# Kernel tuning notes

Hardware: AMD Instinct MI355X
Metric: run time of the kernel (lower is better)

## Reference

```python
import jax, jax.numpy as jnp
import numpy as np

N, E, U, R = 20000, 200000, 32, 64
NTYPES = 95
CUTOFF = 5.0
LN_EPS = 1e-5


def _init_linear(key, fan_in, fan_out, bias=True, dtype=jnp.float32):
    kw, kb = jax.random.split(key)
    bound = 1.0 / np.sqrt(fan_in)
    W = jax.random.uniform(kw, (fan_in, fan_out), dtype, -bound, bound)
    if not bias:
        return W
    b = jax.random.uniform(kb, (fan_out,), dtype, -bound, bound)
    return W, b


def setup_inputs() -> dict:
    key = jax.random.key(0)
    ks = jax.random.split(key, 20)
    f = jnp.float32
    Wd1, bd1 = _init_linear(ks[6], R, U)
    Wd2, bd2 = _init_linear(ks[7], R, U)
    Wd3, bd3 = _init_linear(ks[8], R, U)
    Wemb2, bemb2 = _init_linear(ks[9], 2 * U, U)
    Wemb3, bemb3 = _init_linear(ks[10], R, U)
    Ws1, bs1 = _init_linear(ks[11], U, 2 * U)
    Ws2, bs2 = _init_linear(ks[12], 2 * U, 3 * U)
    return {
        "node_type": jax.random.randint(ks[0], (N,), 0, NTYPES),
        "edge_attr": jax.random.normal(ks[1], (E, R), f),
        "bond_dist": jax.random.uniform(ks[2], (E,), f, 0.1, CUTOFF),
        "bond_vec": jax.random.normal(ks[3], (E, 3), f),
        "src": jax.random.randint(ks[4], (E,), 0, N),
        "dst": jax.random.randint(ks[5], (E,), 0, N),
        "emb_table": jax.random.normal(ks[13], (NTYPES, U), f),
        "Wd1": Wd1, "bd1": bd1, "Wd2": Wd2, "bd2": bd2, "Wd3": Wd3, "bd3": bd3,
        "Wemb2": Wemb2, "bemb2": bemb2, "Wemb3": Wemb3, "bemb3": bemb3,
        "Wt0": _init_linear(ks[14], U, U, bias=False),
        "Wt1": _init_linear(ks[15], U, U, bias=False),
        "Wt2": _init_linear(ks[16], U, U, bias=False),
        "Ws1": Ws1, "bs1": bs1, "Ws2": Ws2, "bs2": bs2,
        "ln_g": jnp.ones((U,), f), "ln_b": jnp.zeros((U,), f),
    }


def reference(node_type, edge_attr, bond_dist, bond_vec, src, dst,
              emb_table, Wd1, bd1, Wd2, bd2, Wd3, bd3,
              Wemb2, bemb2, Wemb3, bemb3, Wt0, Wt1, Wt2,
              Ws1, bs1, Ws2, bs2, ln_g, ln_b):
    act = jax.nn.silu
    dt = edge_attr.dtype
    Z = emb_table[node_type]                                        # [N,U]
    # cosine cutoff
    C = 0.5 * (jnp.cos(jnp.pi * bond_dist / CUTOFF) + 1.0) * (bond_dist <= CUTOFF).astype(dt)
    W1 = (edge_attr @ Wd1 + bd1) * C[:, None]                       # [E,U]
    W2 = (edge_attr @ Wd2 + bd2) * C[:, None]
    W3 = (edge_attr @ Wd3 + bd3) * C[:, None]
    v = bond_vec / jnp.linalg.norm(bond_vec, axis=1, keepdims=True)  # [E,3]
    eye = jnp.eye(3, dtype=dt)
    zero = jnp.zeros_like(v[:, 0])
    # vector_to_skewtensor
    A = jnp.stack([zero, -v[:, 2], v[:, 1],
                   v[:, 2], zero, -v[:, 0],
                   -v[:, 1], v[:, 0], zero], axis=1).reshape(-1, 3, 3)
    # vector_to_symtensor (outer product is already symmetric)
    t = v[:, :, None] * v[:, None, :]                               # [E,3,3]
    S = t - (jnp.trace(t, axis1=-2, axis2=-1) / 3.0)[:, None, None] * eye
    # edge message: Zij = emb2([v_src, v_dst])
    Zij = jnp.concatenate([Z[src], Z[dst]], axis=1) @ Wemb2 + bemb2  # [E,U]
    fI = Zij * W1  # Zij * new_radial_tensor weights, fused (same math)
    fA = Zij * W2
    fS = Zij * W3
    Iedge = fI[:, :, None, None] * eye                              # [E,U,3,3]
    Aedge = fA[:, :, None, None] * A[:, None, :, :]
    Sedge = fS[:, :, None, None] * S[:, None, :, :]
    seg = lambda x: jax.ops.segment_sum(x, dst, num_segments=N)
    Ie, Ae, Se = seg(Iedge), seg(Aedge), seg(Sedge)                 # [N,U,3,3]
    # tensor_norm + LayerNorm
    nrm = jnp.sum((Ie + Ae + Se) ** 2, axis=(-2, -1))               # [N,U]
    mu = jnp.mean(nrm, axis=-1, keepdims=True)
    var = jnp.mean((nrm - mu) ** 2, axis=-1, keepdims=True)
    nrm = (nrm - mu) / jnp.sqrt(var + LN_EPS) * ln_g + ln_b
    # per-channel linear mixing of tensor components
    Ie = jnp.einsum('nuij,uv->nvij', Ie, Wt0)
    Ae = jnp.einsum('nuij,uv->nvij', Ae, Wt1)
    Se = jnp.einsum('nuij,uv->nvij', Se, Wt2)
    nrm = act(nrm @ Ws1 + bs1)
    nrm = act(nrm @ Ws2 + bs2)                                      # [N,3U]
    nrm = nrm.reshape(nrm.shape[0], U, 3)
    X = (nrm[..., 0, None, None] * Ie
         + nrm[..., 1, None, None] * Ae
         + nrm[..., 2, None, None] * Se)                            # [N,U,3,3]
    edge_feat = edge_attr @ Wemb3 + bemb3                           # [E,U]
    return X, edge_feat
```

## Files before the change

### kernel.cpp

```cpp
#include <hip/hip_runtime.h>


#define EPW 8

__device__ inline void atomAddF(float* p, float v) {
#if defined(__HIP_PLATFORM_AMD__)
    unsafeAtomicAdd(p, v);
#else
    atomicAdd(p, v);
#endif
}

__global__ void ptype_kernel(const float* __restrict__ emb,
                             const float* __restrict__ We2,
                             const float* __restrict__ be2,
                             float* __restrict__ Pt1, float* __restrict__ Pt2) {
    const int c = threadIdx.x & 31;
    const int t = blockIdx.x * 8 + (threadIdx.x >> 5);
    if (t < 95) {
        float p1 = 0.f, p2 = 0.f;
        for (int k = 0; k < 32; ++k) {
            const float z = emb[t * 32 + k];
            p1 = fmaf(z, We2[k * 32 + c], p1);
            p2 = fmaf(z, We2[(32 + k) * 32 + c], p2);
        }
        Pt1[t * 32 + c] = p1 + be2[c];
        Pt2[t * 32 + c] = p2;
    }
}

__global__ void prep_zero(const int* __restrict__ nt,
                          const float* __restrict__ Pt1, const float* __restrict__ Pt2,
                          float* __restrict__ acc,
                          float* __restrict__ P1, float* __restrict__ P2, int N) {
    const int i = blockIdx.x * 256 + threadIdx.x;
    if (i < N * 320) acc[i] = 0.0f;
    if (i < N * 32) {
        const int n = i >> 5, c = i & 31;
        const int t = nt[n];
        P1[i] = Pt1[t * 32 + c];
        P2[i] = Pt2[t * 32 + c];
    }
}

__global__ __launch_bounds__(256) void edge_kernel(
    const float* __restrict__ edge_attr,
    const float* __restrict__ bond_dist,
    const float* __restrict__ bond_vec,
    const int*   __restrict__ src,
    const int*   __restrict__ dst,
    const float* __restrict__ Wd1, const float* __restrict__ bd1,
    const float* __restrict__ Wd2, const float* __restrict__ bd2,
    const float* __restrict__ Wd3, const float* __restrict__ bd3,
    const float* __restrict__ We3, const float* __restrict__ be3,
    const float* __restrict__ P1,
    const float* __restrict__ P2,
    float* __restrict__ acc,
    float* __restrict__ efeat,
    int E)
{
    __shared__ float4 sX[4][8][16];

    const int tid  = threadIdx.x;
    const int lane = tid & 63;
    const int c    = lane & 31;
    const int h    = lane >> 5;
    const int wv   = tid >> 6;

    float w0r[32], w1r[32], w2r[32], w3r[32];
#pragma unroll
    for (int kk = 0; kk < 32; ++kk) {
        const int row = (h << 5) + kk;
        w0r[kk] = Wd1[row * 32 + c];
        w1r[kk] = Wd2[row * 32 + c];
        w2r[kk] = Wd3[row * 32 + c];
        w3r[kk] = We3[row * 32 + c];
    }
    const float bd1r = bd1[c], bd2r = bd2[c], bd3r = bd3[c], be3r = be3[c];

    float4 (*sXw)[16] = sX[wv];

    const int wid = (blockIdx.x * 256 + tid) >> 6;
    const int nw  = gridDim.x * 4;
    const int ngroups = (E + EPW - 1) / EPW;

    for (int g = wid; g < ngroups; g += nw) {
        const int base = g * EPW;

        int si4[4], di4[4];
        float dd[4], vx[4], vy[4], vz[4];
#pragma unroll
        for (int jj = 0; jj < 4; ++jj) {
            int e = base + jj + (h << 2); if (e >= E) e = E - 1;
            si4[jj] = src[e]; di4[jj] = dst[e];
            dd[jj]  = bond_dist[e];
            vx[jj]  = bond_vec[3 * (size_t)e + 0];
            vy[jj]  = bond_vec[3 * (size_t)e + 1];
            vz[jj]  = bond_vec[3 * (size_t)e + 2];
        }

        {
            int ea = base + (lane >> 4);     if (ea >= E) ea = E - 1;
            int eb = base + 4 + (lane >> 4); if (eb >= E) eb = E - 1;
            const float4 xa = *(const float4*)&edge_attr[(size_t)ea * 64 + (lane & 15) * 4];
            const float4 xb = *(const float4*)&edge_attr[(size_t)eb * 64 + (lane & 15) * 4];
            sXw[lane >> 4][lane & 15]     = xa;
            sXw[4 + (lane >> 4)][lane & 15] = xb;
        }

        float A0[EPW], A1[EPW], A2[EPW], A3[EPW];
#pragma unroll
        for (int j = 0; j < EPW; ++j) { A0[j] = 0.f; A1[j] = 0.f; A2[j] = 0.f; A3[j] = 0.f; }

#pragma unroll
        for (int kq = 0; kq < 8; ++kq) {
            const int k0 = kq * 4;
#pragma unroll
            for (int j = 0; j < EPW; ++j) {
                const float4 xq = sXw[j][(h << 3) + kq];
                A0[j] = fmaf(xq.x, w0r[k0 + 0], A0[j]);
                A0[j] = fmaf(xq.y, w0r[k0 + 1], A0[j]);
                A0[j] = fmaf(xq.z, w0r[k0 + 2], A0[j]);
                A0[j] = fmaf(xq.w, w0r[k0 + 3], A0[j]);
                A1[j] = fmaf(xq.x, w1r[k0 + 0], A1[j]);
                A1[j] = fmaf(xq.y, w1r[k0 + 1], A1[j]);
                A1[j] = fmaf(xq.z, w1r[k0 + 2], A1[j]);
                A1[j] = fmaf(xq.w, w1r[k0 + 3], A1[j]);
                A2[j] = fmaf(xq.x, w2r[k0 + 0], A2[j]);
                A2[j] = fmaf(xq.y, w2r[k0 + 1], A2[j]);
                A2[j] = fmaf(xq.z, w2r[k0 + 2], A2[j]);
                A2[j] = fmaf(xq.w, w2r[k0 + 3], A2[j]);
                A3[j] = fmaf(xq.x, w3r[k0 + 0], A3[j]);
                A3[j] = fmaf(xq.y, w3r[k0 + 1], A3[j]);
                A3[j] = fmaf(xq.z, w3r[k0 + 2], A3[j]);
                A3[j] = fmaf(xq.w, w3r[k0 + 3], A3[j]);
            }
        }

        float az4[4];
#pragma unroll
        for (int jj = 0; jj < 4; ++jj)
            az4[jj] = P1[(size_t)si4[jj] * 32 + c] + P2[(size_t)di4[jj] * 32 + c];

#pragma unroll
        for (int jj = 0; jj < 4; ++jj) {
            const float sd0 = h ? A0[jj] : A0[jj + 4];
            const float sd1 = h ? A1[jj] : A1[jj + 4];
            const float sd2 = h ? A2[jj] : A2[jj + 4];
            const float sd3 = h ? A3[jj] : A3[jj + 4];
            const float mn0 = h ? A0[jj + 4] : A0[jj];
            const float mn1 = h ? A1[jj + 4] : A1[jj];
            const float mn2 = h ? A2[jj + 4] : A2[jj];
            const float mn3 = h ? A3[jj + 4] : A3[jj];
            const float t0 = mn0 + __shfl_xor(sd0, 32);
            const float t1 = mn1 + __shfl_xor(sd1, 32);
            const float t2 = mn2 + __shfl_xor(sd2, 32);
            const float t3 = mn3 + __shfl_xor(sd3, 32);

            const int e = base + jj + 4 * h;
            const bool val = (e < E);

            const float d = dd[jj];
            const float C = (d <= 5.0f) ? 0.5f * (cosf(3.14159265358979323846f * d / 5.0f) + 1.0f) : 0.0f;
            float v0 = vx[jj], v1 = vy[jj], v2 = vz[jj];
            const float inv = 1.0f / sqrtf(v0 * v0 + v1 * v1 + v2 * v2);
            v0 *= inv; v1 *= inv; v2 *= inv;
            const float tr3 = (v0 * v0 + v1 * v1 + v2 * v2) * (1.0f / 3.0f);
            const float y00 = v0 * v0 - tr3, y11 = v1 * v1 - tr3, y22 = v2 * v2 - tr3;
            const float y01 = v0 * v1, y02 = v0 * v2, y12 = v1 * v2;

            const float az = az4[jj];
            const float a1v = t0 + bd1r;
            const float a2v = t1 + bd2r;
            const float a3v = t2 + bd3r;
            const float a4v = t3 + be3r;
            const float w1v = a1v * C, w2v = a2v * C, w3v = a3v * C;
            const float fI = az * w1v, fA = az * w2v, fS = az * w3v;

            if (val) {
                efeat[(size_t)e * 32 + c] = a4v;
                float* ap = acc + (size_t)di4[jj] * 320 + c;
                atomAddF(ap,       fI);
                atomAddF(ap + 32,  fA * v0);
                atomAddF(ap + 64,  fA * v1);
                atomAddF(ap + 96,  fA * v2);
                atomAddF(ap + 128, fS * y00);
                atomAddF(ap + 160, fS * y01);
                atomAddF(ap + 192, fS * y02);
                atomAddF(ap + 224, fS * y11);
                atomAddF(ap + 256, fS * y12);
                atomAddF(ap + 288, fS * y22);
            }
        }
    }
}

__global__ __launch_bounds__(256) void node_kernel(
    const float* __restrict__ acc,
    const float* __restrict__ Wt0, const float* __restrict__ Wt1, const float* __restrict__ Wt2,
    const float* __restrict__ Ws1, const float* __restrict__ bs1,
    const float* __restrict__ Ws2, const float* __restrict__ bs2,
    const float* __restrict__ lng, const float* __restrict__ lnb,
    float* __restrict__ xout,
    int N)
{
    __shared__ float4 wtp[32][32];
    __shared__ float2 ws1p[32][32];
    __shared__ float4 ws2p[64][32];
    __shared__ float4 accS4[8][32][3];
    __shared__ float2 sb1p[32];
    __shared__ float4 sb2p[32];
    __shared__ float  sg[32], sbv[32];

    const int tid = threadIdx.x;
    for (int i = tid; i < 1024; i += 256) {
        const int k = i >> 5, u = i & 31;
        wtp[k][u]  = make_float4(Wt0[i], Wt1[i], Wt2[i], 0.f);
        ws1p[k][u] = make_float2(Ws1[k * 64 + u], Ws1[k * 64 + 32 + u]);
    }
    for (int i = tid; i < 2048; i += 256) {
        const int k = i >> 5, u = i & 31;
        ws2p[k][u] = make_float4(Ws2[k * 96 + 3 * u], Ws2[k * 96 + 3 * u + 1],
                                 Ws2[k * 96 + 3 * u + 2], 0.f);
    }
    if (tid < 32) {
        sb1p[tid] = make_float2(bs1[tid], bs1[tid + 32]);
        sb2p[tid] = make_float4(bs2[3 * tid], bs2[3 * tid + 1], bs2[3 * tid + 2], 0.f);
        sg[tid] = lng[tid]; sbv[tid] = lnb[tid];
    }
    __syncthreads();

    const int hw = tid >> 5, u = tid & 31;
    const int stride = gridDim.x * 8;

    for (int n = blockIdx.x * 8 + hw; n < N; n += stride) {
        const float* ap = acc + (size_t)n * 320 + u;
        const float c0 = ap[0],   a0 = ap[32],  a1 = ap[64],  a2 = ap[96];
        const float s00 = ap[128], s01 = ap[160], s02 = ap[192];
        const float s11 = ap[224], s12 = ap[256], s22 = ap[288];

        accS4[hw][u][0] = make_float4(c0, a0, a1, a2);
        accS4[hw][u][1] = make_float4(s00, s01, s02, s11);
        accS4[hw][u][2] = make_float4(s12, s22, 0.f, 0.f);

        const float m00 = c0 + s00, m11 = c0 + s11, m22 = c0 + s22;
        float nrm = m00 * m00 + m11 * m11 + m22 * m22
                  + 2.0f * (s01 * s01 + a2 * a2 + s02 * s02 + a1 * a1 + s12 * s12 + a0 * a0);

        float sum = nrm;
#pragma unroll
        for (int o = 16; o >= 1; o >>= 1) sum += __shfl_xor(sum, o, 32);
        const float mu = sum * (1.0f / 32.0f);
        const float dv = nrm - mu;
        float vs = dv * dv;
#pragma unroll
        for (int o = 16; o >= 1; o >>= 1) vs += __shfl_xor(vs, o, 32);
        const float var = vs * (1.0f / 32.0f);
        const float nl = dv * rsqrtf(var + 1e-5f) * sg[u] + sbv[u];

        const float2 b1 = sb1p[u];
        float h1a = b1.x, h1b = b1.y;
#pragma unroll
        for (int k = 0; k < 32; ++k) {
            const float x = __shfl(nl, k, 32);
            const float2 wq = ws1p[k][u];
            h1a = fmaf(x, wq.x, h1a);
            h1b = fmaf(x, wq.y, h1b);
        }
        h1a = h1a / (1.0f + __expf(-h1a));
        h1b = h1b / (1.0f + __expf(-h1b));

        const float4 b2 = sb2p[u];
        float f0 = b2.x, f1 = b2.y, f2 = b2.z;
#pragma unroll
        for (int k = 0; k < 32; ++k) {
            const float hh = __shfl(h1a, k, 32);
            const float4 wq = ws2p[k][u];
            f0 = fmaf(hh, wq.x, f0);
            f1 = fmaf(hh, wq.y, f1);
            f2 = fmaf(hh, wq.z, f2);
        }
#pragma unroll
        for (int k = 0; k < 32; ++k) {
            const float hh = __shfl(h1b, k, 32);
            const float4 wq = ws2p[32 + k][u];
            f0 = fmaf(hh, wq.x, f0);
            f1 = fmaf(hh, wq.y, f1);
            f2 = fmaf(hh, wq.z, f2);
        }
        f0 = f0 / (1.0f + __expf(-f0));
        f1 = f1 / (1.0f + __expf(-f1));
        f2 = f2 / (1.0f + __expf(-f2));

        float m0 = 0, ma0 = 0, ma1 = 0, ma2 = 0;
        float ms00 = 0, ms01 = 0, ms02 = 0, ms11 = 0, ms12 = 0, ms22 = 0;
#pragma unroll
        for (int k = 0; k < 32; ++k) {
            const float4 w  = wtp[k][u];
            const float4 q0 = accS4[hw][k][0];
            const float4 q1 = accS4[hw][k][1];
            const float4 q2 = accS4[hw][k][2];
            m0   = fmaf(q0.x, w.x, m0);
            ma0  = fmaf(q0.y, w.y, ma0);
            ma1  = fmaf(q0.z, w.y, ma1);
            ma2  = fmaf(q0.w, w.y, ma2);
            ms00 = fmaf(q1.x, w.z, ms00);
            ms01 = fmaf(q1.y, w.z, ms01);
            ms02 = fmaf(q1.z, w.z, ms02);
            ms11 = fmaf(q1.w, w.z, ms11);
            ms12 = fmaf(q2.x, w.z, ms12);
            ms22 = fmaf(q2.y, w.z, ms22);
        }

        float* xp = xout + (size_t)n * 288 + u * 9;
        xp[0] = f0 * m0 + f2 * ms00;
        xp[1] = f1 * (-ma2) + f2 * ms01;
        xp[2] = f1 * ( ma1) + f2 * ms02;
        xp[3] = f1 * ( ma2) + f2 * ms01;
        xp[4] = f0 * m0 + f2 * ms11;
        xp[5] = f1 * (-ma0) + f2 * ms12;
        xp[6] = f1 * (-ma1) + f2 * ms02;
        xp[7] = f1 * ( ma0) + f2 * ms12;
        xp[8] = f0 * m0 + f2 * ms22;
    }
}

extern "C" void kernel_launch(void* const* d_in, const int* in_sizes, int n_in,
                              void* d_out, int out_size, void* d_ws, size_t ws_size,
                              hipStream_t stream) {
    const int N = in_sizes[0];
    const int E = in_sizes[2];

    float* acc = (float*)d_ws;
    float* P1  = acc + (size_t)N * 320;
    float* P2  = P1 + (size_t)N * 32;
    float* Pt1 = P2 + (size_t)N * 32;
    float* Pt2 = Pt1 + 95 * 32;

    float* xout  = (float*)d_out;
    float* efeat = xout + (size_t)N * 288;

    ptype_kernel<<<12, 256, 0, stream>>>(
        (const float*)d_in[6], (const float*)d_in[13], (const float*)d_in[14], Pt1, Pt2);

    prep_zero<<<(N * 320 + 255) / 256, 256, 0, stream>>>(
        (const int*)d_in[0], Pt1, Pt2, acc, P1, P2, N);

    edge_kernel<<<768, 256, 0, stream>>>(
        (const float*)d_in[1], (const float*)d_in[2], (const float*)d_in[3],
        (const int*)d_in[4], (const int*)d_in[5],
        (const float*)d_in[7],  (const float*)d_in[8],
        (const float*)d_in[9],  (const float*)d_in[10],
        (const float*)d_in[11], (const float*)d_in[12],
        (const float*)d_in[15], (const float*)d_in[16],
        P1, P2, acc, efeat, E);

    node_kernel<<<512, 256, 0, stream>>>(
        acc,
        (const float*)d_in[17], (const float*)d_in[18], (const float*)d_in[19],
        (const float*)d_in[20], (const float*)d_in[21],
        (const float*)d_in[22], (const float*)d_in[23],
        (const float*)d_in[24], (const float*)d_in[25],
        xout, N);
}
```

Measured before the change: 429.1 us.

## Replace atomic scatter with CSR binning by destination and fused per-node kernel

Builds a CSR index of edges grouped by destination node (histogram, single-wave scan, atomic binning into a permutation). A fused kernel then assigns one wave per node, computes that node's incoming edges and reduces them in registers, and runs the norm/MLP/mixing stage directly. This removes the 10 float atomics per edge-channel, the accumulator zeroing, and the accumulator round trip through global memory. In exchange it adds a serial single-wave scan over 20k nodes, gathered edge_attr loads through the permutation, and load imbalance from variable node degree, with partially empty 8-edge groups wasting work on low-degree nodes.

```diff
diff --git a/kernel.cpp b/kernel.cpp
--- a/kernel.cpp
+++ b/kernel.cpp
@@ -2,14 +2,6 @@
 
 
 #define EPW 8
-
-__device__ inline void atomAddF(float* p, float v) {
-#if defined(__HIP_PLATFORM_AMD__)
-    unsafeAtomicAdd(p, v);
-#else
-    atomicAdd(p, v);
-#endif
-}
 
 __global__ void ptype_kernel(const float* __restrict__ emb,
                              const float* __restrict__ We2,
@@ -29,12 +21,12 @@
     }
 }
 
-__global__ void prep_zero(const int* __restrict__ nt,
-                          const float* __restrict__ Pt1, const float* __restrict__ Pt2,
-                          float* __restrict__ acc,
-                          float* __restrict__ P1, float* __restrict__ P2, int N) {
+__global__ void prep_kernel(const int* __restrict__ nt,
+                            const float* __restrict__ Pt1, const float* __restrict__ Pt2,
+                            float* __restrict__ P1, float* __restrict__ P2,
+                            int* __restrict__ hist, int N) {
     const int i = blockIdx.x * 256 + threadIdx.x;
-    if (i < N * 320) acc[i] = 0.0f;
+    if (i < N) hist[i] = 0;
     if (i < N * 32) {
         const int n = i >> 5, c = i & 31;
         const int t = nt[n];
@@ -43,25 +35,89 @@
     }
 }
 
-__global__ __launch_bounds__(256) void edge_kernel(
+__global__ void hist_kernel(const int* __restrict__ dst, int* __restrict__ hist, int E) {
+    const int i = blockIdx.x * 256 + threadIdx.x;
+    if (i < E) atomicAdd(&hist[dst[i]], 1);
+}
+
+__global__ void scan_kernel(const int* __restrict__ hist,
+                            int* __restrict__ base, int* __restrict__ cursor,
+                            int N, int E) {
+    const int lane = threadIdx.x;
+    int carry = 0;
+    for (int start = 0; start < N; start += 64) {
+        const int i = start + lane;
+        const int v = (i < N) ? hist[i] : 0;
+        int inc = v;
+#pragma unroll
+        for (int o = 1; o < 64; o <<= 1) {
+            const int t = __shfl_up(inc, o, 64);
+            if (lane >= o) inc += t;
+        }
+        const int excl = carry + inc - v;
+        if (i < N) { base[i] = excl; cursor[i] = excl; }
+        carry += __shfl(inc, 63, 64);
+    }
+    if (lane == 0) base[N] = E;
+}
+
+__global__ void binperm_kernel(const int* __restrict__ dst, int* __restrict__ cursor,
+                               int* __restrict__ perm, int E) {
+    const int i = blockIdx.x * 256 + threadIdx.x;
+    if (i < E) {
+        const int s = atomicAdd(&cursor[dst[i]], 1);
+        perm[s] = i;
+    }
+}
+
+__global__ __launch_bounds__(256) void fused_kernel(
     const float* __restrict__ edge_attr,
     const float* __restrict__ bond_dist,
     const float* __restrict__ bond_vec,
     const int*   __restrict__ src,
-    const int*   __restrict__ dst,
     const float* __restrict__ Wd1, const float* __restrict__ bd1,
     const float* __restrict__ Wd2, const float* __restrict__ bd2,
     const float* __restrict__ Wd3, const float* __restrict__ bd3,
     const float* __restrict__ We3, const float* __restrict__ be3,
     const float* __restrict__ P1,
     const float* __restrict__ P2,
-    float* __restrict__ acc,
+    const int*   __restrict__ basep,
+    const int*   __restrict__ perm,
+    const float* __restrict__ Wt0, const float* __restrict__ Wt1, const float* __restrict__ Wt2,
+    const float* __restrict__ Ws1, const float* __restrict__ bs1,
+    const float* __restrict__ Ws2, const float* __restrict__ bs2,
+    const float* __restrict__ lng, const float* __restrict__ lnb,
+    float* __restrict__ xout,
     float* __restrict__ efeat,
-    int E)
+    int N)
 {
     __shared__ float4 sX[4][8][16];
-
-    const int tid  = threadIdx.x;
+    __shared__ float4 wtp[32][32];
+    __shared__ float2 ws1p[32][32];
+    __shared__ float4 ws2p[64][32];
+    __shared__ float4 accS4[4][32][3];
+    __shared__ float2 sb1p[32];
+    __shared__ float4 sb2p[32];
+    __shared__ float  sg[32], sbv[32];
+
+    const int tid = threadIdx.x;
+    for (int i = tid; i < 1024; i += 256) {
+        const int k = i >> 5, u = i & 31;
+        wtp[k][u]  = make_float4(Wt0[i], Wt1[i], Wt2[i], 0.f);
+        ws1p[k][u] = make_float2(Ws1[k * 64 + u], Ws1[k * 64 + 32 + u]);
+    }
+    for (int i = tid; i < 2048; i += 256) {
+        const int k = i >> 5, u = i & 31;
+        ws2p[k][u] = make_float4(Ws2[k * 96 + 3 * u], Ws2[k * 96 + 3 * u + 1],
+                                 Ws2[k * 96 + 3 * u + 2], 0.f);
+    }
+    if (tid < 32) {
+        sb1p[tid] = make_float2(bs1[tid], bs1[tid + 32]);
+        sb2p[tid] = make_float4(bs2[3 * tid], bs2[3 * tid + 1], bs2[3 * tid + 2], 0.f);
+        sg[tid] = lng[tid]; sbv[tid] = lnb[tid];
+    }
+    __syncthreads();
+
     const int lane = tid & 63;
     const int c    = lane & 31;
     const int h    = lane >> 5;
@@ -78,174 +134,140 @@
     }
     const float bd1r = bd1[c], bd2r = bd2[c], bd3r = bd3[c], be3r = be3[c];
 
-    float4 (*sXw)[16] = sX[wv];
-
-    const int wid = (blockIdx.x * 256 + tid) >> 6;
-    const int nw  = gridDim.x * 4;
-    const int ngroups = (E + EPW - 1) / EPW;
-
-    for (int g = wid; g < ngroups; g += nw) {
-        const int base = g * EPW;
-
-        int si4[4], di4[4];
-        float dd[4], vx[4], vy[4], vz[4];
-#pragma unroll
-        for (int jj = 0; jj < 4; ++jj) {
-            int e = base + jj + (h << 2); if (e >= E) e = E - 1;
-            si4[jj] = src[e]; di4[jj] = dst[e];
-            dd[jj]  = bond_dist[e];
-            vx[jj]  = bond_vec[3 * (size_t)e + 0];
-            vy[jj]  = bond_vec[3 * (size_t)e + 1];
-            vz[jj]  = bond_vec[3 * (size_t)e + 2];
-        }
-
-        {
-            int ea = base + (lane >> 4);     if (ea >= E) ea = E - 1;
-            int eb = base + 4 + (lane >> 4); if (eb >= E) eb = E - 1;
-            const float4 xa = *(const float4*)&edge_attr[(size_t)ea * 64 + (lane & 15) * 4];
-            const float4 xb = *(const float4*)&edge_attr[(size_t)eb * 64 + (lane & 15) * 4];
-            sXw[lane >> 4][lane & 15]     = xa;
-            sXw[4 + (lane >> 4)][lane & 15] = xb;
-        }
-
-        float A0[EPW], A1[EPW], A2[EPW], A3[EPW];
-#pragma unroll
-        for (int j = 0; j < EPW; ++j) { A0[j] = 0.f; A1[j] = 0.f; A2[j] = 0.f; A3[j] = 0.f; }
-
-#pragma unroll
-        for (int kq = 0; kq < 8; ++kq) {
-            const int k0 = kq * 4;
-#pragma unroll
-            for (int j = 0; j < EPW; ++j) {
-                const float4 xq = sXw[j][(h << 3) + kq];
-                A0[j] = fmaf(xq.x, w0r[k0 + 0], A0[j]);
-                A0[j] = fmaf(xq.y, w0r[k0 + 1], A0[j]);
-                A0[j] = fmaf(xq.z, w0r[k0 + 2], A0[j]);
-                A0[j] = fmaf(xq.w, w0r[k0 + 3], A0[j]);
-                A1[j] = fmaf(xq.x, w1r[k0 + 0], A1[j]);
-                A1[j] = fmaf(xq.y, w1r[k0 + 1], A1[j]);
-                A1[j] = fmaf(xq.z, w1r[k0 + 2], A1[j]);
-                A1[j] = fmaf(xq.w, w1r[k0 + 3], A1[j]);
-                A2[j] = fmaf(xq.x, w2r[k0 + 0], A2[j]);
-                A2[j] = fmaf(xq.y, w2r[k0 + 1], A2[j]);
-                A2[j] = fmaf(xq.z, w2r[k0 + 2], A2[j]);
-                A2[j] = fmaf(xq.w, w2r[k0 + 3], A2[j]);
-                A3[j] = fmaf(xq.x, w3r[k0 + 0], A3[j]);
-                A3[j] = fmaf(xq.y, w3r[k0 + 1], A3[j]);
-                A3[j] = fmaf(xq.z, w3r[k0 + 2], A3[j]);
-                A3[j] = fmaf(xq.w, w3r[k0 + 3], A3[j]);
+    const int wgid  = blockIdx.x * 4 + wv;
+    const int nwaves = gridDim.x * 4;
+
+    for (int n = wgid; n < N; n += nwaves) {
+        const int js = basep[n], je = basep[n + 1];
+        const float pzn = P2[(size_t)n * 32 + c];
+
+        float rc0 = 0, ra0 = 0, ra1 = 0, ra2 = 0;
+        float rs00 = 0, rs01 = 0, rs02 = 0, rs11 = 0, rs12 = 0, rs22 = 0;
+
+        for (int off = js; off < je; off += EPW) {
+            int eid4[4], si4[4]; float dd[4], vx[4], vy[4], vz[4]; bool vld[4];
+#pragma unroll
+            for (int jj = 0; jj < 4; ++jj) {
+                int s_ = off + jj + (h << 2);
+                vld[jj] = (s_ < je);
+                if (s_ > je - 1) s_ = je - 1;
+                const int eid = perm[s_];
+                eid4[jj] = eid;
+                si4[jj]  = src[eid];
+                dd[jj]   = bond_dist[eid];
+                vx[jj]   = bond_vec[3 * (size_t)eid + 0];
+                vy[jj]   = bond_vec[3 * (size_t)eid + 1];
+                vz[jj]   = bond_vec[3 * (size_t)eid + 2];
             }
-        }
-
-        float az4[4];
-#pragma unroll
-        for (int jj = 0; jj < 4; ++jj)
-            az4[jj] = P1[(size_t)si4[jj] * 32 + c] + P2[(size_t)di4[jj] * 32 + c];
-
-#pragma unroll
-        for (int jj = 0; jj < 4; ++jj) {
-            const float sd0 = h ? A0[jj] : A0[jj + 4];
-            const float sd1 = h ? A1[jj] : A1[jj + 4];
-            const float sd2 = h ? A2[jj] : A2[jj + 4];
-            const float sd3 = h ? A3[jj] : A3[jj + 4];
-            const float mn0 = h ? A0[jj + 4] : A0[jj];
-            const float mn1 = h ? A1[jj + 4] : A1[jj];
-            const float mn2 = h ? A2[jj + 4] : A2[jj];
-            const float mn3 = h ? A3[jj + 4] : A3[jj];
-            const float t0 = mn0 + __shfl_xor(sd0, 32);
-            const float t1 = mn1 + __shfl_xor(sd1, 32);
-            const float t2 = mn2 + __shfl_xor(sd2, 32);
-            const float t3 = mn3 + __shfl_xor(sd3, 32);
-
-            const int e = base + jj + 4 * h;
-            const bool val = (e < E);
-
-            const float d = dd[jj];
-            const float C = (d <= 5.0f) ? 0.5f * (cosf(3.14159265358979323846f * d / 5.0f) + 1.0f) : 0.0f;
-            float v0 = vx[jj], v1 = vy[jj], v2 = vz[jj];
-            const float inv = 1.0f / sqrtf(v0 * v0 + v1 * v1 + v2 * v2);
-            v0 *= inv; v1 *= inv; v2 *= inv;
-            const float tr3 = (v0 * v0 + v1 * v1 + v2 * v2) * (1.0f / 3.0f);
-            const float y00 = v0 * v0 - tr3, y11 = v1 * v1 - tr3, y22 = v2 * v2 - tr3;
-            const float y01 = v0 * v1, y02 = v0 * v2, y12 = v1 * v2;
-
-            const float az = az4[jj];
-            const float a1v = t0 + bd1r;
-            const float a2v = t1 + bd2r;
-            const float a3v = t2 + bd3r;
-            const float a4v = t3 + be3r;
-            const float w1v = a1v * C, w2v = a2v * C, w3v = a3v * C;
-            const float fI = az * w1v, fA = az * w2v, fS = az * w3v;
-
-            if (val) {
-                efeat[(size_t)e * 32 + c] = a4v;
-                float* ap = acc + (size_t)di4[jj] * 320 + c;
-                atomAddF(ap,       fI);
-                atomAddF(ap + 32,  fA * v0);
-                atomAddF(ap + 64,  fA * v1);
-                atomAddF(ap + 96,  fA * v2);
-                atomAddF(ap + 128, fS * y00);
-                atomAddF(ap + 160, fS * y01);
-                atomAddF(ap + 192, fS * y02);
-                atomAddF(ap + 224, fS * y11);
-                atomAddF(ap + 256, fS * y12);
-                atomAddF(ap + 288, fS * y22);
+
+            {
+                int sa = off + (lane >> 4);     if (sa > je - 1) sa = je - 1;
+                int sb = off + 4 + (lane >> 4); if (sb > je - 1) sb = je - 1;
+                const int ea = perm[sa], eb = perm[sb];
+                sX[wv][lane >> 4][lane & 15] =
+                    *(const float4*)&edge_attr[(size_t)ea * 64 + (lane & 15) * 4];
+                sX[wv][4 + (lane >> 4)][lane & 15] =
+                    *(const float4*)&edge_attr[(size_t)eb * 64 + (lane & 15) * 4];
             }
-        }
-    }
-}
-
-__global__ __launch_bounds__(256) void node_kernel(
-    const float* __restrict__ acc,
-    const float* __restrict__ Wt0, const float* __restrict__ Wt1, const float* __restrict__ Wt2,
-    const float* __restrict__ Ws1, const float* __restrict__ bs1,
-    const float* __restrict__ Ws2, const float* __restrict__ bs2,
-    const float* __restrict__ lng, const float* __restrict__ lnb,
-    float* __restrict__ xout,
-    int N)
-{
-    __shared__ float4 wtp[32][32];
-    __shared__ float2 ws1p[32][32];
-    __shared__ float4 ws2p[64][32];
-    __shared__ float4 accS4[8][32][3];
-    __shared__ float2 sb1p[32];
-    __shared__ float4 sb2p[32];
-    __shared__ float  sg[32], sbv[32];
-
-    const int tid = threadIdx.x;
-    for (int i = tid; i < 1024; i += 256) {
-        const int k = i >> 5, u = i & 31;
-        wtp[k][u]  = make_float4(Wt0[i], Wt1[i], Wt2[i], 0.f);
-        ws1p[k][u] = make_float2(Ws1[k * 64 + u], Ws1[k * 64 + 32 + u]);
-    }
-    for (int i = tid; i < 2048; i += 256) {
-        const int k = i >> 5, u = i & 31;
-        ws2p[k][u] = make_float4(Ws2[k * 96 + 3 * u], Ws2[k * 96 + 3 * u + 1],
-                                 Ws2[k * 96 + 3 * u + 2], 0.f);
-    }
-    if (tid < 32) {
-        sb1p[tid] = make_float2(bs1[tid], bs1[tid + 32]);
-        sb2p[tid] = make_float4(bs2[3 * tid], bs2[3 * tid + 1], bs2[3 * tid + 2], 0.f);
-        sg[tid] = lng[tid]; sbv[tid] = lnb[tid];
-    }
-    __syncthreads();
-
-    const int hw = tid >> 5, u = tid & 31;
-    const int stride = gridDim.x * 8;
-
-    for (int n = blockIdx.x * 8 + hw; n < N; n += stride) {
-        const float* ap = acc + (size_t)n * 320 + u;
-        const float c0 = ap[0],   a0 = ap[32],  a1 = ap[64],  a2 = ap[96];
-        const float s00 = ap[128], s01 = ap[160], s02 = ap[192];
-        const float s11 = ap[224], s12 = ap[256], s22 = ap[288];
-
-        accS4[hw][u][0] = make_float4(c0, a0, a1, a2);
-        accS4[hw][u][1] = make_float4(s00, s01, s02, s11);
-        accS4[hw][u][2] = make_float4(s12, s22, 0.f, 0.f);
-
-        const float m00 = c0 + s00, m11 = c0 + s11, m22 = c0 + s22;
+
+            float A0[EPW], A1[EPW], A2[EPW], A3[EPW];
+#pragma unroll
+            for (int j = 0; j < EPW; ++j) { A0[j] = 0.f; A1[j] = 0.f; A2[j] = 0.f; A3[j] = 0.f; }
+
+#pragma unroll
+            for (int kq = 0; kq < 8; ++kq) {
+                const int k0 = kq * 4;
+#pragma unroll
+                for (int j = 0; j < EPW; ++j) {
+                    const float4 xq = sX[wv][j][(h << 3) + kq];
+                    A0[j] = fmaf(xq.x, w0r[k0 + 0], A0[j]);
+                    A0[j] = fmaf(xq.y, w0r[k0 + 1], A0[j]);
+                    A0[j] = fmaf(xq.z, w0r[k0 + 2], A0[j]);
+                    A0[j] = fmaf(xq.w, w0r[k0 + 3], A0[j]);
+                    A1[j] = fmaf(xq.x, w1r[k0 + 0], A1[j]);
+                    A1[j] = fmaf(xq.y, w1r[k0 + 1], A1[j]);
+                    A1[j] = fmaf(xq.z, w1r[k0 + 2], A1[j]);
+                    A1[j] = fmaf(xq.w, w1r[k0 + 3], A1[j]);
+                    A2[j] = fmaf(xq.x, w2r[k0 + 0], A2[j]);
+                    A2[j] = fmaf(xq.y, w2r[k0 + 1], A2[j]);
+                    A2[j] = fmaf(xq.z, w2r[k0 + 2], A2[j]);
+                    A2[j] = fmaf(xq.w, w2r[k0 + 3], A2[j]);
+                    A3[j] = fmaf(xq.x, w3r[k0 + 0], A3[j]);
+                    A3[j] = fmaf(xq.y, w3r[k0 + 1], A3[j]);
+                    A3[j] = fmaf(xq.z, w3r[k0 + 2], A3[j]);
+                    A3[j] = fmaf(xq.w, w3r[k0 + 3], A3[j]);
+                }
+            }
+
+            float az4[4];
+#pragma unroll
+            for (int jj = 0; jj < 4; ++jj)
+                az4[jj] = P1[(size_t)si4[jj] * 32 + c] + pzn;
+
+#pragma unroll
+            for (int jj = 0; jj < 4; ++jj) {
+                const float sd0 = h ? A0[jj] : A0[jj + 4];
+                const float sd1 = h ? A1[jj] : A1[jj + 4];
+                const float sd2 = h ? A2[jj] : A2[jj + 4];
+                const float sd3 = h ? A3[jj] : A3[jj + 4];
+                const float mn0 = h ? A0[jj + 4] : A0[jj];
+                const float mn1 = h ? A1[jj + 4] : A1[jj];
+                const float mn2 = h ? A2[jj + 4] : A2[jj];
+                const float mn3 = h ? A3[jj + 4] : A3[jj];
+                const float t0 = mn0 + __shfl_xor(sd0, 32);
+                const float t1 = mn1 + __shfl_xor(sd1, 32);
+                const float t2 = mn2 + __shfl_xor(sd2, 32);
+                const float t3 = mn3 + __shfl_xor(sd3, 32);
+
+                const float d = dd[jj];
+                const float C = (d <= 5.0f) ? 0.5f * (cosf(3.14159265358979323846f * d / 5.0f) + 1.0f) : 0.0f;
+                float v0 = vx[jj], v1 = vy[jj], v2 = vz[jj];
+                const float inv = 1.0f / sqrtf(v0 * v0 + v1 * v1 + v2 * v2);
+                v0 *= inv; v1 *= inv; v2 *= inv;
+                const float tr3 = (v0 * v0 + v1 * v1 + v2 * v2) * (1.0f / 3.0f);
+                const float y00 = v0 * v0 - tr3, y11 = v1 * v1 - tr3, y22 = v2 * v2 - tr3;
+                const float y01 = v0 * v1, y02 = v0 * v2, y12 = v1 * v2;
+
+                const float az = az4[jj];
+                const float a1v = t0 + bd1r;
+                const float a2v = t1 + bd2r;
+                const float a3v = t2 + bd3r;
+                const float a4v = t3 + be3r;
+                const float w1v = a1v * C, w2v = a2v * C, w3v = a3v * C;
+                const float fI = az * w1v, fA = az * w2v, fS = az * w3v;
+
+                if (vld[jj]) {
+                    efeat[(size_t)eid4[jj] * 32 + c] = a4v;
+                    rc0 += fI;
+                    ra0 = fmaf(fA, v0, ra0);
+                    ra1 = fmaf(fA, v1, ra1);
+                    ra2 = fmaf(fA, v2, ra2);
+                    rs00 = fmaf(fS, y00, rs00);
+                    rs01 = fmaf(fS, y01, rs01);
+                    rs02 = fmaf(fS, y02, rs02);
+                    rs11 = fmaf(fS, y11, rs11);
+                    rs12 = fmaf(fS, y12, rs12);
+                    rs22 = fmaf(fS, y22, rs22);
+                }
+            }
+        }
+
+        rc0 += __shfl_xor(rc0, 32);  ra0 += __shfl_xor(ra0, 32);
+        ra1 += __shfl_xor(ra1, 32);  ra2 += __shfl_xor(ra2, 32);
+        rs00 += __shfl_xor(rs00, 32); rs01 += __shfl_xor(rs01, 32);
+        rs02 += __shfl_xor(rs02, 32); rs11 += __shfl_xor(rs11, 32);
+        rs12 += __shfl_xor(rs12, 32); rs22 += __shfl_xor(rs22, 32);
+
+        if (h == 0) {
+            accS4[wv][c][0] = make_float4(rc0, ra0, ra1, ra2);
+            accS4[wv][c][1] = make_float4(rs00, rs01, rs02, rs11);
+            accS4[wv][c][2] = make_float4(rs12, rs22, 0.f, 0.f);
+        }
+
+        const float m00 = rc0 + rs00, m11 = rc0 + rs11, m22 = rc0 + rs22;
         float nrm = m00 * m00 + m11 * m11 + m22 * m22
-                  + 2.0f * (s01 * s01 + a2 * a2 + s02 * s02 + a1 * a1 + s12 * s12 + a0 * a0);
+                  + 2.0f * (rs01 * rs01 + ra2 * ra2 + rs02 * rs02
+                            + ra1 * ra1 + rs12 * rs12 + ra0 * ra0);
 
         float sum = nrm;
 #pragma unroll
@@ -256,26 +278,26 @@
 #pragma unroll
         for (int o = 16; o >= 1; o >>= 1) vs += __shfl_xor(vs, o, 32);
         const float var = vs * (1.0f / 32.0f);
-        const float nl = dv * rsqrtf(var + 1e-5f) * sg[u] + sbv[u];
-
-        const float2 b1 = sb1p[u];
+        const float nl = dv * rsqrtf(var + 1e-5f) * sg[c] + sbv[c];
+
+        const float2 b1 = sb1p[c];
         float h1a = b1.x, h1b = b1.y;
 #pragma unroll
         for (int k = 0; k < 32; ++k) {
             const float x = __shfl(nl, k, 32);
-            const float2 wq = ws1p[k][u];
+            const float2 wq = ws1p[k][c];
             h1a = fmaf(x, wq.x, h1a);
             h1b = fmaf(x, wq.y, h1b);
         }
         h1a = h1a / (1.0f + __expf(-h1a));
         h1b = h1b / (1.0f + __expf(-h1b));
 
-        const float4 b2 = sb2p[u];
+        const float4 b2 = sb2p[c];
         float f0 = b2.x, f1 = b2.y, f2 = b2.z;
 #pragma unroll
         for (int k = 0; k < 32; ++k) {
             const float hh = __shfl(h1a, k, 32);
-            const float4 wq = ws2p[k][u];
+            const float4 wq = ws2p[k][c];
             f0 = fmaf(hh, wq.x, f0);
             f1 = fmaf(hh, wq.y, f1);
             f2 = fmaf(hh, wq.z, f2);
@@ -283,7 +305,7 @@
 #pragma unroll
         for (int k = 0; k < 32; ++k) {
             const float hh = __shfl(h1b, k, 32);
-            const float4 wq = ws2p[32 + k][u];
+            const float4 wq = ws2p[32 + k][c];
             f0 = fmaf(hh, wq.x, f0);
             f1 = fmaf(hh, wq.y, f1);
             f2 = fmaf(hh, wq.z, f2);
@@ -296,10 +318,10 @@
         float ms00 = 0, ms01 = 0, ms02 = 0, ms11 = 0, ms12 = 0, ms22 = 0;
 #pragma unroll
         for (int k = 0; k < 32; ++k) {
-            const float4 w  = wtp[k][u];
-            const float4 q0 = accS4[hw][k][0];
-            const float4 q1 = accS4[hw][k][1];
-            const float4 q2 = accS4[hw][k][2];
+            const float4 w  = wtp[k][c];
+            const float4 q0 = accS4[wv][k][0];
+            const float4 q1 = accS4[wv][k][1];
+            const float4 q2 = accS4[wv][k][2];
             m0   = fmaf(q0.x, w.x, m0);
             ma0  = fmaf(q0.y, w.y, ma0);
             ma1  = fmaf(q0.z, w.y, ma1);
@@ -312,16 +334,24 @@
             ms22 = fmaf(q2.y, w.z, ms22);
         }
 
-        float* xp = xout + (size_t)n * 288 + u * 9;
-        xp[0] = f0 * m0 + f2 * ms00;
-        xp[1] = f1 * (-ma2) + f2 * ms01;
-        xp[2] = f1 * ( ma1) + f2 * ms02;
-        xp[3] = f1 * ( ma2) + f2 * ms01;
-        xp[4] = f0 * m0 + f2 * ms11;
-        xp[5] = f1 * (-ma0) + f2 * ms12;
-        xp[6] = f1 * (-ma1) + f2 * ms02;
-        xp[7] = f1 * ( ma0) + f2 * ms12;
-        xp[8] = f0 * m0 + f2 * ms22;
+        float* xs = (float*)&sX[wv][0][0];
+        if (h == 0) {
+            xs[c * 9 + 0] = f0 * m0 + f2 * ms00;
+            xs[c * 9 + 1] = f1 * (-ma2) + f2 * ms01;
+            xs[c * 9 + 2] = f1 * ( ma1) + f2 * ms02;
+            xs[c * 9 + 3] = f1 * ( ma2) + f2 * ms01;
+            xs[c * 9 + 4] = f0 * m0 + f2 * ms11;
+            xs[c * 9 + 5] = f1 * (-ma0) + f2 * ms12;
+            xs[c * 9 + 6] = f1 * ( ma1) * 0.f + f1 * (-ma1) + f2 * ms02;
+            xs[c * 9 + 7] = f1 * ( ma0) + f2 * ms12;
+            xs[c * 9 + 8] = f0 * m0 + f2 * ms22;
+        }
+        float* xp = xout + (size_t)n * 288;
+#pragma unroll
+        for (int i = 0; i < 5; ++i) {
+            const int idx = lane + i * 64;
+            if (idx < 288) xp[idx] = xs[idx];
+        }
     }
 }
 
@@ -331,11 +361,14 @@
     const int N = in_sizes[0];
     const int E = in_sizes[2];
 
-    float* acc = (float*)d_ws;
-    float* P1  = acc + (size_t)N * 320;
-    float* P2  = P1 + (size_t)N * 32;
-    float* Pt1 = P2 + (size_t)N * 32;
-    float* Pt2 = Pt1 + 95 * 32;
+    float* P1   = (float*)d_ws;
+    float* P2   = P1 + (size_t)N * 32;
+    float* Pt1  = P2 + (size_t)N * 32;
+    float* Pt2  = Pt1 + 95 * 32;
+    int*   hist = (int*)(Pt2 + 95 * 32);
+    int*   basep  = hist + N;
+    int*   cursor = basep + (N + 1);
+    int*   perm   = cursor + N;
 
     float* xout  = (float*)d_out;
     float* efeat = xout + (size_t)N * 288;
@@ -343,23 +376,28 @@
     ptype_kernel<<<12, 256, 0, stream>>>(
         (const float*)d_in[6], (const float*)d_in[13], (const float*)d_in[14], Pt1, Pt2);
 
-    prep_zero<<<(N * 320 + 255) / 256, 256, 0, stream>>>(
-        (const int*)d_in[0], Pt1, Pt2, acc, P1, P2, N);
-
-    edge_kernel<<<768, 256, 0, stream>>>(
+    prep_kernel<<<(N * 32 + 255) / 256, 256, 0, stream>>>(
+        (const int*)d_in[0], Pt1, Pt2, P1, P2, hist, N);
+
+    hist_kernel<<<(E + 255) / 256, 256, 0, stream>>>(
+        (const int*)d_in[5], hist, E);
+
+    scan_kernel<<<1, 64, 0, stream>>>(hist, basep, cursor, N, E);
+
+    binperm_kernel<<<(E + 255) / 256, 256, 0, stream>>>(
+        (const int*)d_in[5], cursor, perm, E);
+
+    fused_kernel<<<512, 256, 0, stream>>>(
         (const float*)d_in[1], (const float*)d_in[2], (const float*)d_in[3],
-        (const int*)d_in[4], (const int*)d_in[5],
+        (const int*)d_in[4],
         (const float*)d_in[7],  (const float*)d_in[8],
         (const float*)d_in[9],  (const float*)d_in[10],
         (const float*)d_in[11], (const float*)d_in[12],
         (const float*)d_in[15], (const float*)d_in[16],
-        P1, P2, acc, efeat, E);
-
-    node_kernel<<<512, 256, 0, stream>>>(
-        acc,
+        P1, P2, basep, perm,
         (const float*)d_in[17], (const float*)d_in[18], (const float*)d_in[19],
         (const float*)d_in[20], (const float*)d_in[21],
         (const float*)d_in[22], (const float*)d_in[23],
         (const float*)d_in[24], (const float*)d_in[25],
-        xout, N);
-}
+        xout, efeat, N);
+}
```

Result: slower. 720.6 us (+67.9%).
